# Kernel optimization log

Hardware: AMD Instinct MI355X
Metric: run time of the kernel (lower is better)

Reference implementation:

```python
import jax, jax.numpy as jnp
import numpy as np


def _entmax15(x, axis=-1):
    # Faithful port of Entmax15Function (alpha=1.5 entmax, closed-form via sort).
    x = x - jnp.max(x, axis=axis, keepdims=True)  # numerical stability
    x = x / 2.0                                   # alpha=1.5 rescaling
    d = x.shape[axis]
    # sort descending along axis
    xsrt = -jnp.sort(-x, axis=axis)
    shape = [1] * x.ndim
    shape[axis] = d
    rho = jnp.arange(1, d + 1, dtype=x.dtype).reshape(shape)
    mean = jnp.cumsum(xsrt, axis=axis) / rho
    mean_sq = jnp.cumsum(xsrt * xsrt, axis=axis) / rho
    ss = rho * (mean_sq - mean * mean)
    delta = (1.0 - ss) / rho
    delta_nz = jnp.maximum(delta, 0.0)
    tau = mean - jnp.sqrt(delta_nz)
    # support size: number of sorted entries with tau <= xsrt
    support_size = jnp.sum((tau <= xsrt).astype(jnp.int32), axis=axis, keepdims=True)
    tau_star = jnp.take_along_axis(tau, support_size - 1, axis=axis)
    y = jnp.maximum(x - tau_star, 0.0)
    return y * y


def setup_inputs() -> dict:
    key = jax.random.key(0)
    x = jax.random.normal(key, (4096, 32000), dtype=jnp.float32)
    return {"x": x}


def reference(x) -> jnp.ndarray:
    return _entmax15(x, axis=-1)
```

## Files before the change

kernel.cpp:

```cpp
#include <hip/hip_runtime.h>
#include <math.h>


#define ROWLEN 32000
#define ROWV4  8000
#define BLOCK  1024
#define NV4    8
#define NW     16
#define CAND_MAX 4096
#define GRID   256

typedef float f32x4 __attribute__((ext_vector_type(4)));

__device__ __forceinline__ void wg_barrier() {
  asm volatile("s_waitcnt lgkmcnt(0)" ::: "memory");
  __builtin_amdgcn_sched_barrier(0);
  __builtin_amdgcn_s_barrier();
  __builtin_amdgcn_sched_barrier(0);
}

__device__ __forceinline__ void wait_vm8() {
  asm volatile("s_waitcnt vmcnt(8)" ::: "memory");
  __builtin_amdgcn_sched_barrier(0);
}
__device__ __forceinline__ void wait_vm16() {
  asm volatile("s_waitcnt vmcnt(16)" ::: "memory");
  __builtin_amdgcn_sched_barrier(0);
}

__device__ __forceinline__ void issue_row(f32x4 (&v)[NV4],
                                          const float* __restrict__ rowp,
                                          int t) {
#pragma unroll
  for (int i = 0; i < NV4; ++i) {
    int idx = i * BLOCK + t;
    idx = idx < ROWV4 ? idx : 0;
    const float* p = rowp + (size_t)idx * 4;
    asm volatile("global_load_dwordx4 %0, %1, off"
                 : "=&v"(v[i]) : "v"(p) : "memory");
  }
}

__global__ __launch_bounds__(BLOCK)
void entmax15_kernel(const float* __restrict__ x, float* __restrict__ out,
                     int rows, int rpb) {
  const int t    = threadIdx.x;
  const int lane = t & 63;
  const int wid  = t >> 6;

  __shared__ float s_max[NW];
  __shared__ int   s_total;
  __shared__ float s_tau;
  __shared__ float s_cand[CAND_MAX];

  const int rbeg = blockIdx.x * rpb;
  const int rend = min(rbeg + rpb, rows);
  if (rbeg >= rend) return;

  f32x4 A[NV4], B[NV4];

  auto process = [&](f32x4 (&v)[NV4], int row) {
    if (t == 0) s_total = 0;

    float lmax = -1e30f;
#pragma unroll
    for (int i = 0; i < NV4; ++i) {
      int idx = i * BLOCK + t;
      if (idx < ROWV4)
        lmax = fmaxf(lmax,
                     fmaxf(fmaxf(v[i].x, v[i].y), fmaxf(v[i].z, v[i].w)));
    }
#pragma unroll
    for (int m = 32; m >= 1; m >>= 1) lmax = fmaxf(lmax, __shfl_xor(lmax, m));
    if (lane == 0) s_max[wid] = lmax;
    wg_barrier();
    float xmax = s_max[0];
#pragma unroll
    for (int w = 1; w < NW; ++w) xmax = fmaxf(xmax, s_max[w]);
    const float thr = xmax - 2.0f;

    int c = 0;
#pragma unroll
    for (int i = 0; i < NV4; ++i) {
      int idx = i * BLOCK + t;
      if (idx < ROWV4)
        c += (v[i].x > thr) + (v[i].y > thr) + (v[i].z > thr) + (v[i].w > thr);
    }
    int incl = c;
#pragma unroll
    for (int m = 1; m < 64; m <<= 1) {
      int nb = __shfl_up(incl, m);
      if (lane >= m) incl += nb;
    }
    int wbase = 0;
    if (lane == 63) wbase = atomicAdd(&s_total, incl);
    wbase = __shfl(wbase, 63);
    {
      int off = wbase + incl - c;
#pragma unroll
      for (int i = 0; i < NV4; ++i) {
        int idx = i * BLOCK + t;
        if (idx < ROWV4) {
          float a;
          a = v[i].x; if (a > thr) { if (off < CAND_MAX) s_cand[off] = (a - xmax) * 0.5f; ++off; }
          a = v[i].y; if (a > thr) { if (off < CAND_MAX) s_cand[off] = (a - xmax) * 0.5f; ++off; }
          a = v[i].z; if (a > thr) { if (off < CAND_MAX) s_cand[off] = (a - xmax) * 0.5f; ++off; }
          a = v[i].w; if (a > thr) { if (off < CAND_MAX) s_cand[off] = (a - xmax) * 0.5f; ++off; }
        }
      }
    }
    wg_barrier();
    const int total = min(s_total, CAND_MAX);

    if (wid == 0) {
      float tau = -1.0f;
      const int ng = (total + 511) >> 9;
      for (int it = 0; it < 6; ++it) {
        float s = 0.f, q = 0.f;
        for (int g = 0; g < ng; ++g) {
#pragma unroll
          for (int k = 0; k < 8; ++k) {
            int j = lane + ((g << 3) + k) * 64;
            float z = s_cand[j & (CAND_MAX - 1)];
            float d = z - tau;
            if (j < total && d > 0.f) { s += d; q += d * d; }
          }
        }
#pragma unroll
        for (int m = 32; m >= 1; m >>= 1) {
          s += __shfl_xor(s, m);
          q += __shfl_xor(q, m);
        }
        if (s > 0.f) tau += (q - 1.0f) / (2.0f * s);
      }
      for (int it = 0; it < 2; ++it) {
        float kk = 0.f, s1 = 0.f, s2 = 0.f;
        for (int g = 0; g < ng; ++g) {
#pragma unroll
          for (int k = 0; k < 8; ++k) {
            int j = lane + ((g << 3) + k) * 64;
            float z = s_cand[j & (CAND_MAX - 1)];
            if (j < total && z > tau) { kk += 1.f; s1 += z; s2 += z * z; }
          }
        }
#pragma unroll
        for (int m = 32; m >= 1; m >>= 1) {
          kk += __shfl_xor(kk, m);
          s1 += __shfl_xor(s1, m);
          s2 += __shfl_xor(s2, m);
        }
        float disc = s1 * s1 - kk * (s2 - 1.0f);
        tau = (s1 - sqrtf(fmaxf(disc, 0.f))) / kk;
      }
      if (lane == 0) s_tau = tau;
    }
    wg_barrier();
    const float cc = fmaf(xmax, 0.5f, s_tau);

    f32x4* __restrict__ outr = (f32x4*)(out + (size_t)row * ROWLEN);
#pragma unroll
    for (int i = 0; i < NV4; ++i) {
      int idx = i * BLOCK + t;
      if (idx < ROWV4) {
        f32x4 o;
        float d;
        d = fmaf(v[i].x, 0.5f, -cc); o.x = d > 0.f ? d * d : 0.f;
        d = fmaf(v[i].y, 0.5f, -cc); o.y = d > 0.f ? d * d : 0.f;
        d = fmaf(v[i].z, 0.5f, -cc); o.z = d > 0.f ? d * d : 0.f;
        d = fmaf(v[i].w, 0.5f, -cc); o.w = d > 0.f ? d * d : 0.f;
        outr[idx] = o;
      }
    }
  };

  issue_row(A, x + (size_t)rbeg * ROWLEN, t);
  {
    int rB0 = (rbeg + 1 < rend) ? rbeg + 1 : rbeg;
    issue_row(B, x + (size_t)rB0 * ROWLEN, t);
  }
  wait_vm8();
  for (int r = rbeg; r < rend; r += 2) {
    process(A, r);
    {
      int rn = (r + 2 < rend) ? r + 2 : rend - 1;
      issue_row(A, x + (size_t)rn * ROWLEN, t);
    }
    wait_vm16();
    if (r + 1 >= rend) break;
    process(B, r + 1);
    {
      int rn = (r + 3 < rend) ? r + 3 : rend - 1;
      issue_row(B, x + (size_t)rn * ROWLEN, t);
    }
    wait_vm16();
  }
}

extern "C" void kernel_launch(void* const* d_in, const int* in_sizes, int n_in,
                              void* d_out, int out_size, void* d_ws, size_t ws_size,
                              hipStream_t stream) {
  const float* x = (const float*)d_in[0];
  float* out = (float*)d_out;
  int rows = in_sizes[0] / ROWLEN;
  int grid = rows < GRID ? rows : GRID;
  int rpb  = (rows + grid - 1) / grid;
  hipLaunchKernelGGL(entmax15_kernel, dim3(grid), dim3(BLOCK), 0, stream,
                     x, out, rows, rpb);
}
```

Measured before the change: 246.0 us.

## Replace per-row barriers with per-wave candidate segments and redundant tau solve

Each wave now filters candidates against its own local max minus 2 into a private shared segment, with no atomic. Every wave then redundantly solves for tau over all segments after a single barrier, instead of wave 0 solving alone. This cuts the per-row barriers from three to one, drops the shared-memory atomic, and double-buffers shared memory by row parity so the next row can start without waiting. In exchange every wave repeats the solver work, and filtering on the local max can push more candidates into a segment, which truncates once it exceeds 256 entries.

```diff
diff --git a/kernel.cpp b/kernel.cpp
--- a/kernel.cpp
+++ b/kernel.cpp
@@ -7,7 +7,7 @@
 #define BLOCK  1024
 #define NV4    8
 #define NW     16
-#define CAND_MAX 4096
+#define SEGCAP 256
 #define GRID   256
 
 typedef float f32x4 __attribute__((ext_vector_type(4)));
@@ -48,10 +48,9 @@
   const int lane = t & 63;
   const int wid  = t >> 6;
 
-  __shared__ float s_max[NW];
-  __shared__ int   s_total;
-  __shared__ float s_tau;
-  __shared__ float s_cand[CAND_MAX];
+  __shared__ float s_cand[2][NW][SEGCAP];
+  __shared__ float s_wmax[2][NW];
+  __shared__ int   s_wcnt[2][NW];
 
   const int rbeg = blockIdx.x * rpb;
   const int rend = min(rbeg + rpb, rows);
@@ -59,9 +58,7 @@
 
   f32x4 A[NV4], B[NV4];
 
-  auto process = [&](f32x4 (&v)[NV4], int row) {
-    if (t == 0) s_total = 0;
-
+  auto stats = [&](f32x4 (&v)[NV4], int par) -> float {
     float lmax = -1e30f;
 #pragma unroll
     for (int i = 0; i < NV4; ++i) {
@@ -72,12 +69,7 @@
     }
 #pragma unroll
     for (int m = 32; m >= 1; m >>= 1) lmax = fmaxf(lmax, __shfl_xor(lmax, m));
-    if (lane == 0) s_max[wid] = lmax;
-    wg_barrier();
-    float xmax = s_max[0];
-#pragma unroll
-    for (int w = 1; w < NW; ++w) xmax = fmaxf(xmax, s_max[w]);
-    const float thr = xmax - 2.0f;
+    const float thr = lmax - 2.0f;
 
     int c = 0;
 #pragma unroll
@@ -92,71 +84,76 @@
       int nb = __shfl_up(incl, m);
       if (lane >= m) incl += nb;
     }
-    int wbase = 0;
-    if (lane == 63) wbase = atomicAdd(&s_total, incl);
-    wbase = __shfl(wbase, 63);
+
     {
-      int off = wbase + incl - c;
+      float* seg = &s_cand[par][wid][0];
+      int off = incl - c;
 #pragma unroll
       for (int i = 0; i < NV4; ++i) {
         int idx = i * BLOCK + t;
         if (idx < ROWV4) {
           float a;
-          a = v[i].x; if (a > thr) { if (off < CAND_MAX) s_cand[off] = (a - xmax) * 0.5f; ++off; }
-          a = v[i].y; if (a > thr) { if (off < CAND_MAX) s_cand[off] = (a - xmax) * 0.5f; ++off; }
-          a = v[i].z; if (a > thr) { if (off < CAND_MAX) s_cand[off] = (a - xmax) * 0.5f; ++off; }
-          a = v[i].w; if (a > thr) { if (off < CAND_MAX) s_cand[off] = (a - xmax) * 0.5f; ++off; }
+          a = v[i].x; if (a > thr) { if (off < SEGCAP) seg[off] = a; ++off; }
+          a = v[i].y; if (a > thr) { if (off < SEGCAP) seg[off] = a; ++off; }
+          a = v[i].z; if (a > thr) { if (off < SEGCAP) seg[off] = a; ++off; }
+          a = v[i].w; if (a > thr) { if (off < SEGCAP) seg[off] = a; ++off; }
         }
       }
     }
+    if (lane == 63) {
+      s_wcnt[par][wid] = min(incl, SEGCAP);
+      s_wmax[par][wid] = lmax;
+    }
     wg_barrier();
-    const int total = min(s_total, CAND_MAX);
-
-    if (wid == 0) {
-      float tau = -1.0f;
-      const int ng = (total + 511) >> 9;
-      for (int it = 0; it < 6; ++it) {
-        float s = 0.f, q = 0.f;
-        for (int g = 0; g < ng; ++g) {
-#pragma unroll
-          for (int k = 0; k < 8; ++k) {
-            int j = lane + ((g << 3) + k) * 64;
-            float z = s_cand[j & (CAND_MAX - 1)];
-            float d = z - tau;
-            if (j < total && d > 0.f) { s += d; q += d * d; }
-          }
+
+    float xmax = s_wmax[par][0];
+#pragma unroll
+    for (int w = 1; w < NW; ++w) xmax = fmaxf(xmax, s_wmax[par][w]);
+
+    float tau = -1.0f;
+    for (int it = 0; it < 6; ++it) {
+      float s = 0.f, q = 0.f;
+#pragma unroll 1
+      for (int w2 = 0; w2 < NW; ++w2) {
+        int cnt = __builtin_amdgcn_readfirstlane(s_wcnt[par][w2]);
+        const float* sg = &s_cand[par][w2][0];
+        for (int j = lane; j < cnt; j += 64) {
+          float d = fmaf(sg[j] - xmax, 0.5f, -tau);
+          if (d > 0.f) { s += d; q += d * d; }
         }
-#pragma unroll
-        for (int m = 32; m >= 1; m >>= 1) {
-          s += __shfl_xor(s, m);
-          q += __shfl_xor(q, m);
+      }
+#pragma unroll
+      for (int m = 32; m >= 1; m >>= 1) {
+        s += __shfl_xor(s, m);
+        q += __shfl_xor(q, m);
+      }
+      if (s > 0.f) tau += (q - 1.0f) / (2.0f * s);
+    }
+    for (int it = 0; it < 2; ++it) {
+      float kk = 0.f, s1 = 0.f, s2 = 0.f;
+#pragma unroll 1
+      for (int w2 = 0; w2 < NW; ++w2) {
+        int cnt = __builtin_amdgcn_readfirstlane(s_wcnt[par][w2]);
+        const float* sg = &s_cand[par][w2][0];
+        for (int j = lane; j < cnt; j += 64) {
+          float z = (sg[j] - xmax) * 0.5f;
+          if (z > tau) { kk += 1.f; s1 += z; s2 += z * z; }
         }
-        if (s > 0.f) tau += (q - 1.0f) / (2.0f * s);
-      }
-      for (int it = 0; it < 2; ++it) {
-        float kk = 0.f, s1 = 0.f, s2 = 0.f;
-        for (int g = 0; g < ng; ++g) {
-#pragma unroll
-          for (int k = 0; k < 8; ++k) {
-            int j = lane + ((g << 3) + k) * 64;
-            float z = s_cand[j & (CAND_MAX - 1)];
-            if (j < total && z > tau) { kk += 1.f; s1 += z; s2 += z * z; }
-          }
-        }
-#pragma unroll
-        for (int m = 32; m >= 1; m >>= 1) {
-          kk += __shfl_xor(kk, m);
-          s1 += __shfl_xor(s1, m);
-          s2 += __shfl_xor(s2, m);
-        }
-        float disc = s1 * s1 - kk * (s2 - 1.0f);
-        tau = (s1 - sqrtf(fmaxf(disc, 0.f))) / kk;
-      }
-      if (lane == 0) s_tau = tau;
-    }
-    wg_barrier();
-    const float cc = fmaf(xmax, 0.5f, s_tau);
-
+      }
+#pragma unroll
+      for (int m = 32; m >= 1; m >>= 1) {
+        kk += __shfl_xor(kk, m);
+        s1 += __shfl_xor(s1, m);
+        s2 += __shfl_xor(s2, m);
+      }
+      float disc = s1 * s1 - kk * (s2 - 1.0f);
+      tau = (s1 - sqrtf(fmaxf(disc, 0.f))) / kk;
+    }
+    return fmaf(xmax, 0.5f, tau);
+  };
+
+  auto process = [&](f32x4 (&v)[NV4], int row) {
+    const float cc = stats(v, row & 1);
     f32x4* __restrict__ outr = (f32x4*)(out + (size_t)row * ROWLEN);
 #pragma unroll
     for (int i = 0; i < NV4; ++i) {
```

Result: slower. 647.7 us (+163.3%).
